# Kernel optimization log

Hardware: AMD Instinct MI355X
Metric: run time of the kernel (lower is better)

## Reference

```python
import jax, jax.numpy as jnp
import numpy as np

B, T, F, H = 256, 32, 128, 128
NUM_FILTERS, KH, KW, NUM_CLASSES = 64, 2, 2, 2
FLAT = NUM_FILTERS * (T - KH + 1) * (2 * F - KW + 1)  # 64*31*255 = 505920


def setup_inputs() -> dict:
    key = jax.random.key(0)
    ks = jax.random.split(key, 12)
    inp = {
        "X_nume": jax.random.normal(ks[0], (B, T, F), jnp.float32),
        "att_W": jax.random.uniform(ks[1], (F, H), jnp.float32),
        "att_U": jax.random.uniform(ks[2], (F, H), jnp.float32),
        "att_V": jax.random.uniform(ks[3], (H, 1), jnp.float32),
        "conv_w": jax.random.normal(ks[4], (NUM_FILTERS, 1, KH, KW), jnp.float32) * 0.5,
        "conv_b": jax.random.normal(ks[5], (NUM_FILTERS,), jnp.float32) * 0.1,
        "w1": jax.random.normal(ks[6], (FLAT, 256), jnp.float32) * (1.0 / np.sqrt(FLAT)),
        "b1": jnp.zeros((256,), jnp.float32),
        "w2": jax.random.normal(ks[7], (256, 32), jnp.float32) * (1.0 / np.sqrt(256)),
        "b2": jnp.zeros((32,), jnp.float32),
        "w3": jax.random.normal(ks[8], (32, NUM_CLASSES), jnp.float32) * (1.0 / np.sqrt(32)),
        "b3": jnp.zeros((NUM_CLASSES,), jnp.float32),
    }
    return inp


def reference(X_nume, att_W, att_U, att_V, conv_w, conv_b, w1, b1, w2, b2, w3, b3):
    X = X_nume  # [B, T, F]
    # --- additive attention, fully batched (replaces O(T^2) python loops) ---
    xw = jnp.einsum("btf,fh->bth", X, att_W)  # query proj [B,T,H]
    xu = jnp.einsum("btf,fh->bth", X, att_U)  # key proj   [B,T,H]
    # e[b,i,j] = V^T tanh(x_i W + x_j U)
    scores = jnp.squeeze(jnp.tanh(xw[:, :, None, :] + xu[:, None, :, :]) @ att_V, -1)  # [B,T,T]
    alpha = jax.nn.softmax(scores, axis=-1)  # softmax over j (includes diagonal)
    # context excludes j == i (original skips j == index AFTER softmax)
    mask = 1.0 - jnp.eye(T, dtype=X.dtype)
    c = jnp.einsum("bij,bjf->bif", alpha * mask, X)  # [B,T,F]
    feat = jnp.concatenate([X, c], axis=-1)  # [B,T,2F]
    # --- conv ---
    conv_in = feat[:, None, :, :]  # [B,1,T,2F]
    conv = jax.lax.conv_general_dilated(
        conv_in, conv_w, window_strides=(1, 1), padding="VALID",
        dimension_numbers=("NCHW", "OIHW", "NCHW"))
    conv = jax.nn.relu(conv + conv_b[None, :, None, None])  # [B,64,T-1,2F-1]
    # --- MLP head ---
    flat = conv.reshape(conv.shape[0], -1)
    h = jax.nn.relu(flat @ w1 + b1)
    h = jax.nn.relu(h @ w2 + b2)
    return h @ w3 + b3
```

## Files before the change

### kernel.cpp

```cpp
#include <hip/hip_runtime.h>
#include <hip/hip_bf16.h>

#define B_ 256
#define T_ 32
#define F_ 128
#define H_ 128
#define NF 64
#define OH 31
#define OW 255
#define POS_TOTAL (OH*OW)
#define N1 256
#define KT 248

typedef __attribute__((ext_vector_type(8))) short bf16x8;
typedef __attribute__((ext_vector_type(4))) float f32x4;

__device__ __forceinline__ unsigned int cvtpk(float lo, float hi) {
    unsigned int r;
    asm("v_cvt_pk_bf16_f32 %0, %1, %2" : "=v"(r) : "v"(lo), "v"(hi));
    return r;
}

__global__ __launch_bounds__(256) void k_attn(
    const float* __restrict__ X, const float* __restrict__ W,
    const float* __restrict__ U, const float* __restrict__ V,
    float* __restrict__ featL)
{
    __shared__ float Xs[T_][F_];
    __shared__ float xw[T_][H_];
    __shared__ float xu[T_][H_];
    __shared__ float sc[T_][T_];
    __shared__ float Vs[H_];

    const int b = blockIdx.x;
    const int t = threadIdx.x;
    const float* Xb = X + (size_t)b * T_ * F_;

    for (int idx = t; idx < T_*F_; idx += 256) ((float*)Xs)[idx] = Xb[idx];
    if (t < H_) Vs[t] = V[t];
    __syncthreads();

    {
        const int h = t & 127, half = t >> 7;
        float aw[16], au[16];
        #pragma unroll
        for (int r = 0; r < 16; r++) { aw[r] = 0.f; au[r] = 0.f; }
        for (int f = 0; f < F_; f++) {
            const float wv = W[f*H_ + h];
            const float uv = U[f*H_ + h];
            #pragma unroll
            for (int r = 0; r < 16; r++) {
                const float xv = Xs[half*16 + r][f];
                aw[r] += xv * wv;
                au[r] += xv * uv;
            }
        }
        #pragma unroll
        for (int r = 0; r < 16; r++) {
            xw[half*16 + r][h] = aw[r];
            xu[half*16 + r][h] = au[r];
        }
    }
    __syncthreads();

    {
        const int i = t >> 3;
        const int j0 = (t & 7) * 4;
        float s0 = 0.f, s1 = 0.f, s2 = 0.f, s3 = 0.f;
        for (int h = 0; h < H_; h++) {
            const float xwv = xw[i][h];
            const float vv  = Vs[h];
            s0 += tanhf(xwv + xu[j0+0][h]) * vv;
            s1 += tanhf(xwv + xu[j0+1][h]) * vv;
            s2 += tanhf(xwv + xu[j0+2][h]) * vv;
            s3 += tanhf(xwv + xu[j0+3][h]) * vv;
        }
        sc[i][j0+0] = s0; sc[i][j0+1] = s1; sc[i][j0+2] = s2; sc[i][j0+3] = s3;
    }
    __syncthreads();

    if (t < T_) {
        float m = -1e30f;
        #pragma unroll
        for (int j = 0; j < T_; j++) m = fmaxf(m, sc[t][j]);
        float sum = 0.f;
        #pragma unroll
        for (int j = 0; j < T_; j++) sum += expf(sc[t][j] - m);
        const float inv = 1.f / sum;
        #pragma unroll
        for (int j = 0; j < T_; j++) {
            const float a = expf(sc[t][j] - m) * inv;
            sc[t][j] = (j == t) ? 0.f : a;
        }
    }
    __syncthreads();

    for (int idx = t; idx < T_*F_; idx += 256) {
        const int row = idx >> 7, f = idx & 127;
        float acc = 0.f;
        #pragma unroll
        for (int j = 0; j < T_; j++) acc += sc[row][j] * Xs[j][f];
        float* fr = featL + (size_t)b*8192 + row*256;
        fr[f]       = Xs[row][f];
        fr[128 + f] = acc;
    }
}

__global__ __launch_bounds__(256) void k_tr(
    const float* __restrict__ src, float* __restrict__ dst)
{
    __shared__ float tile[32][33];
    const int rc0 = blockIdx.x * 32;
    const int b0  = blockIdx.y * 32;
    const int tx = threadIdx.x & 31;
    const int ty = threadIdx.x >> 5;
    #pragma unroll
    for (int r = 0; r < 32; r += 8)
        tile[ty + r][tx] = src[(size_t)(b0 + ty + r)*8192 + rc0 + tx];
    __syncthreads();
    #pragma unroll
    for (int r = 0; r < 32; r += 8)
        dst[(size_t)(rc0 + ty + r)*256 + b0 + tx] = tile[tx][ty + r];
}

__global__ __launch_bounds__(512, 2) void k_gemm1(
    const float* __restrict__ featT, const float* __restrict__ cw,
    const float* __restrict__ cb, const float* __restrict__ w1,
    float* __restrict__ partial)
{
    __shared__ unsigned short As[2][256*64];
    __shared__ unsigned short Ws[2][256*64];
    __shared__ float cwL[256];
    __shared__ float cbL[64];

    const int t  = threadIdx.x;
    const int kt = blockIdx.x;
    const int y  = kt >> 3;
    const int x0 = (kt & 7) * 32;

    if (t < 256) cwL[t] = cw[t];
    if (t < 64)  cbL[t] = cb[t];

    const int rm = t & 255;
    const int ph = t >> 8;
    const int r0 = (t & 15) * 4;
    const int c0 = (t >> 4) * 8;
    const int lane = t & 63, wid = t >> 6;
    const int wm = (wid >> 2) * 128;
    const int wn = (wid & 3) * 64;
    const int fr = lane & 15, fq = lane >> 4;

    f32x4 acc[8][4];
    #pragma unroll
    for (int i = 0; i < 8; i++)
        #pragma unroll
        for (int j = 0; j < 4; j++)
            acc[i][j] = (f32x4){0.f, 0.f, 0.f, 0.f};

    float topv[17], botv[17];
    #pragma unroll
    for (int i = 0; i < 17; i++) {
        int xc = x0 + ph*16 + i; if (xc > 255) xc = 255;
        topv[i] = featT[((size_t)(y*256 + xc))*256 + rm];
        botv[i] = featT[((size_t)((y+1)*256 + xc))*256 + rm];
    }

    float wvf[4][8];

#define W_LOADS(S)                                                             \
    {                                                                          \
        const int fl_ = r0 >> 5;                                               \
        const int f_  = 2*(S) + fl_;                                           \
        _Pragma("unroll")                                                      \
        for (int jj = 0; jj < 4; jj++) {                                       \
            int xc_ = x0 + (r0 & 31) + jj; if (xc_ > 254) xc_ = 254;           \
            const float* wp_ = w1 + ((size_t)(f_*POS_TOTAL + y*255 + xc_))*N1  \
                                  + c0;                                        \
            *(float4*)&wvf[jj][0] = *(const float4*)&wp_[0];                   \
            *(float4*)&wvf[jj][4] = *(const float4*)&wp_[4];                   \
        }                                                                      \
    }

#define STAGE(BUF, S)                                                          \
    {                                                                          \
        _Pragma("unroll")                                                      \
        for (int i = 0; i < 8; i++) {                                          \
            const int n_ = c0 + i;                                             \
            uint2 v_;                                                          \
            v_.x = cvtpk(wvf[0][i], wvf[1][i]);                                \
            v_.y = cvtpk(wvf[2][i], wvf[3][i]);                                \
            const int blk_ = (r0 >> 3) ^ (n_ & 7);                             \
            *(uint2*)&Ws[BUF][n_*64 + blk_*8 + (r0 & 7)] = v_;                 \
        }                                                                      \
        _Pragma("unroll")                                                      \
        for (int fl = 0; fl < 2; fl++) {                                       \
            const int f_ = 2*(S) + fl;                                         \
            const float4 cc_ = *(const float4*)&cwL[f_*4];                     \
            const float cbv_ = cbL[f_];                                        \
            unsigned int pk_[4];                                               \
            _Pragma("unroll")                                                  \
            for (int i2 = 0; i2 < 8; i2++) {                                   \
                const int i0 = 2*i2, i1 = 2*i2 + 1;                            \
                float v0_ = topv[i0]*cc_.x + topv[i0+1]*cc_.y                  \
                          + botv[i0]*cc_.z + botv[i0+1]*cc_.w + cbv_;          \
                float v1_ = topv[i1]*cc_.x + topv[i1+1]*cc_.y                  \
                          + botv[i1]*cc_.z + botv[i1+1]*cc_.w + cbv_;          \
                v0_ = (x0 + ph*16 + i0 < 255) ? fmaxf(v0_, 0.f) : 0.f;         \
                v1_ = (x0 + ph*16 + i1 < 255) ? fmaxf(v1_, 0.f) : 0.f;         \
                pk_[i2 & 3] = cvtpk(v0_, v1_);                                 \
                if ((i2 & 3) == 3) {                                           \
                    const int kb_ = fl*4 + ph*2 + (i2 >> 2);                   \
                    *(uint4*)&As[BUF][rm*64 + ((kb_ ^ (rm & 7))*8)]            \
                        = *(uint4*)&pk_[0];                                    \
                }                                                              \
            }                                                                  \
        }                                                                      \
    }

    W_LOADS(0);
    __syncthreads();
    STAGE(0, 0);
    asm volatile("s_waitcnt lgkmcnt(0)" ::: "memory");
    __builtin_amdgcn_s_barrier();

    #pragma unroll 1
    for (int s = 0; s < 32; s++) {
        const int cur = s & 1;
        if (s < 31) W_LOADS(s + 1);

        __builtin_amdgcn_s_setprio(1);
        #pragma unroll
        for (int kc = 0; kc < 2; kc++) {
            const int sw = ((kc*4 + fq) ^ (fr & 7)) * 8;
            bf16x8 bf_[4];
            #pragma unroll
            for (int ng = 0; ng < 4; ng++)
                bf_[ng] = *(const bf16x8*)&Ws[cur][(wn + ng*16 + fr)*64 + sw];
            #pragma unroll
            for (int mg = 0; mg < 8; mg++) {
                const bf16x8 af_ =
                    *(const bf16x8*)&As[cur][(wm + mg*16 + fr)*64 + sw];
                #pragma unroll
                for (int ng = 0; ng < 4; ng++)
                    acc[mg][ng] = __builtin_amdgcn_mfma_f32_16x16x32_bf16(
                        af_, bf_[ng], acc[mg][ng], 0, 0, 0);
            }
        }
        __builtin_amdgcn_s_setprio(0);

        if (s < 31) STAGE(cur ^ 1, s + 1);
        asm volatile("s_waitcnt lgkmcnt(0)" ::: "memory");
        __builtin_amdgcn_s_barrier();
    }

    float* pp = partial + (size_t)kt * (256*N1);
    #pragma unroll
    for (int mg = 0; mg < 8; mg++)
        #pragma unroll
        for (int ng = 0; ng < 4; ng++) {
            const int col = wn + ng*16 + fr;
            #pragma unroll
            for (int j = 0; j < 4; j++) {
                const int row = wm + mg*16 + fq*4 + j;
                pp[(size_t)row*N1 + col] = acc[mg][ng][j];
            }
        }
#undef W_LOADS
#undef STAGE
}

__global__ __launch_bounds__(256) void k_head(
    const float* __restrict__ partial,
    const float* __restrict__ b1, const float* __restrict__ w2,
    const float* __restrict__ b2, const float* __restrict__ w3,
    const float* __restrict__ b3, float* __restrict__ out)
{
    __shared__ float h1s[256];
    __shared__ float h2s[32];
    const int b = blockIdx.x, t = threadIdx.x;

    const float* pb = partial + (size_t)b*N1 + t;
    float s0 = 0.f, s1 = 0.f, s2 = 0.f, s3 = 0.f;
    #pragma unroll 2
    for (int kt = 0; kt < KT; kt += 4) {
        s0 += pb[(size_t)(kt+0)*65536];
        s1 += pb[(size_t)(kt+1)*65536];
        s2 += pb[(size_t)(kt+2)*65536];
        s3 += pb[(size_t)(kt+3)*65536];
    }
    h1s[t] = fmaxf(b1[t] + ((s0+s1)+(s2+s3)), 0.f);
    __syncthreads();

    if (t < 32) {
        float s2v = b2[t];
        for (int i = 0; i < 256; i++) s2v += h1s[i] * w2[i*32 + t];
        h2s[t] = fmaxf(s2v, 0.f);
    }
    __syncthreads();

    if (t < 2) {
        float s3v = b3[t];
        #pragma unroll
        for (int i = 0; i < 32; i++) s3v += h2s[i] * w3[i*2 + t];
        out[b*2 + t] = s3v;
    }
}

extern "C" void kernel_launch(void* const* d_in, const int* in_sizes, int n_in,
                              void* d_out, int out_size, void* d_ws, size_t ws_size,
                              hipStream_t stream) {
    const float* X    = (const float*)d_in[0];
    const float* attW = (const float*)d_in[1];
    const float* attU = (const float*)d_in[2];
    const float* attV = (const float*)d_in[3];
    const float* cw   = (const float*)d_in[4];
    const float* cb   = (const float*)d_in[5];
    const float* w1   = (const float*)d_in[6];
    const float* b1   = (const float*)d_in[7];
    const float* w2   = (const float*)d_in[8];
    const float* b2   = (const float*)d_in[9];
    const float* w3   = (const float*)d_in[10];
    const float* b3   = (const float*)d_in[11];
    float* out = (float*)d_out;

    float* featL   = (float*)d_ws;
    float* featT   = (float*)((char*)d_ws + (8u<<20));
    float* partial = (float*)((char*)d_ws + (16u<<20));

    k_attn <<<dim3(B_),       dim3(256), 0, stream>>>(X, attW, attU, attV, featL);
    k_tr   <<<dim3(256, 8),   dim3(256), 0, stream>>>(featL, featT);
    k_gemm1<<<dim3(KT),       dim3(512), 0, stream>>>(featT, cw, cb, w1, partial);
    k_head <<<dim3(B_),       dim3(256), 0, stream>>>(partial, b1, w2, b2, w3, b3, out);
}
```

Baseline: 269.5 us.

## Load w1 fragments straight into registers and drop the LDS weight buffer

```diff
diff --git a/kernel.cpp b/kernel.cpp
--- a/kernel.cpp
+++ b/kernel.cpp
@@ -129,7 +129,6 @@
     float* __restrict__ partial)
 {
     __shared__ unsigned short As[2][256*64];
-    __shared__ unsigned short Ws[2][256*64];
     __shared__ float cwL[256];
     __shared__ float cbL[64];
 
@@ -143,19 +142,16 @@
 
     const int rm = t & 255;
     const int ph = t >> 8;
-    const int r0 = (t & 15) * 4;
-    const int c0 = (t >> 4) * 8;
     const int lane = t & 63, wid = t >> 6;
-    const int wm = (wid >> 2) * 128;
-    const int wn = (wid & 3) * 64;
+    const int wn = wid * 32;
     const int fr = lane & 15, fq = lane >> 4;
 
-    f32x4 acc[8][4];
-    #pragma unroll
-    for (int i = 0; i < 8; i++)
-        #pragma unroll
-        for (int j = 0; j < 4; j++)
-            acc[i][j] = (f32x4){0.f, 0.f, 0.f, 0.f};
+    f32x4 acc[16][2];
+    #pragma unroll
+    for (int i = 0; i < 16; i++) {
+        acc[i][0] = (f32x4){0.f, 0.f, 0.f, 0.f};
+        acc[i][1] = (f32x4){0.f, 0.f, 0.f, 0.f};
+    }
 
     float topv[17], botv[17];
     #pragma unroll
@@ -165,33 +161,30 @@
         botv[i] = featT[((size_t)((y+1)*256 + xc))*256 + rm];
     }
 
-    float wvf[4][8];
-
-#define W_LOADS(S)                                                             \
+    int poff[8];
+    #pragma unroll
+    for (int j = 0; j < 8; j++) {
+        int xc = x0 + fq*8 + j; if (xc > 254) xc = 254;
+        poff[j] = (y*255 + xc)*N1 + wn + fr;
+    }
+
+    float wv[2][2][8];
+
+#define WLOAD(S)                                                               \
     {                                                                          \
-        const int fl_ = r0 >> 5;                                               \
-        const int f_  = 2*(S) + fl_;                                           \
         _Pragma("unroll")                                                      \
-        for (int jj = 0; jj < 4; jj++) {                                       \
-            int xc_ = x0 + (r0 & 31) + jj; if (xc_ > 254) xc_ = 254;           \
-            const float* wp_ = w1 + ((size_t)(f_*POS_TOTAL + y*255 + xc_))*N1  \
-                                  + c0;                                        \
-            *(float4*)&wvf[jj][0] = *(const float4*)&wp_[0];                   \
-            *(float4*)&wvf[jj][4] = *(const float4*)&wp_[4];                   \
+        for (int kc = 0; kc < 2; kc++) {                                       \
+            const float* wf_ = w1 + (size_t)(2*(S) + kc) * (POS_TOTAL*N1);     \
+            _Pragma("unroll")                                                  \
+            for (int ng = 0; ng < 2; ng++)                                     \
+                _Pragma("unroll")                                              \
+                for (int j = 0; j < 8; j++)                                    \
+                    wv[kc][ng][j] = wf_[poff[j] + ng*16];                      \
         }                                                                      \
     }
 
 #define STAGE(BUF, S)                                                          \
     {                                                                          \
-        _Pragma("unroll")                                                      \
-        for (int i = 0; i < 8; i++) {                                          \
-            const int n_ = c0 + i;                                             \
-            uint2 v_;                                                          \
-            v_.x = cvtpk(wvf[0][i], wvf[1][i]);                                \
-            v_.y = cvtpk(wvf[2][i], wvf[3][i]);                                \
-            const int blk_ = (r0 >> 3) ^ (n_ & 7);                             \
-            *(uint2*)&Ws[BUF][n_*64 + blk_*8 + (r0 & 7)] = v_;                 \
-        }                                                                      \
         _Pragma("unroll")                                                      \
         for (int fl = 0; fl < 2; fl++) {                                       \
             const int f_ = 2*(S) + fl;                                         \
@@ -217,7 +210,7 @@
         }                                                                      \
     }
 
-    W_LOADS(0);
+    WLOAD(0);
     __syncthreads();
     STAGE(0, 0);
     asm volatile("s_waitcnt lgkmcnt(0)" ::: "memory");
@@ -226,24 +219,32 @@
     #pragma unroll 1
     for (int s = 0; s < 32; s++) {
         const int cur = s & 1;
-        if (s < 31) W_LOADS(s + 1);
+
+        bf16x8 bf[2][2];
+        #pragma unroll
+        for (int kc = 0; kc < 2; kc++)
+            #pragma unroll
+            for (int ng = 0; ng < 2; ng++) {
+                unsigned int* bu = (unsigned int*)&bf[kc][ng];
+                #pragma unroll
+                for (int q = 0; q < 4; q++)
+                    bu[q] = cvtpk(wv[kc][ng][2*q], wv[kc][ng][2*q+1]);
+            }
+
+        if (s < 31) WLOAD(s + 1);
 
         __builtin_amdgcn_s_setprio(1);
         #pragma unroll
         for (int kc = 0; kc < 2; kc++) {
             const int sw = ((kc*4 + fq) ^ (fr & 7)) * 8;
-            bf16x8 bf_[4];
             #pragma unroll
-            for (int ng = 0; ng < 4; ng++)
-                bf_[ng] = *(const bf16x8*)&Ws[cur][(wn + ng*16 + fr)*64 + sw];
-            #pragma unroll
-            for (int mg = 0; mg < 8; mg++) {
-                const bf16x8 af_ =
-                    *(const bf16x8*)&As[cur][(wm + mg*16 + fr)*64 + sw];
-                #pragma unroll
-                for (int ng = 0; ng < 4; ng++)
-                    acc[mg][ng] = __builtin_amdgcn_mfma_f32_16x16x32_bf16(
-                        af_, bf_[ng], acc[mg][ng], 0, 0, 0);
+            for (int mg = 0; mg < 16; mg++) {
+                const bf16x8 af =
+                    *(const bf16x8*)&As[cur][(mg*16 + fr)*64 + sw];
+                acc[mg][0] = __builtin_amdgcn_mfma_f32_16x16x32_bf16(
+                    af, bf[kc][0], acc[mg][0], 0, 0, 0);
+                acc[mg][1] = __builtin_amdgcn_mfma_f32_16x16x32_bf16(
+                    af, bf[kc][1], acc[mg][1], 0, 0, 0);
             }
         }
         __builtin_amdgcn_s_setprio(0);
@@ -255,17 +256,17 @@
 
     float* pp = partial + (size_t)kt * (256*N1);
     #pragma unroll
-    for (int mg = 0; mg < 8; mg++)
-        #pragma unroll
-        for (int ng = 0; ng < 4; ng++) {
+    for (int mg = 0; mg < 16; mg++)
+        #pragma unroll
+        for (int ng = 0; ng < 2; ng++) {
             const int col = wn + ng*16 + fr;
             #pragma unroll
             for (int j = 0; j < 4; j++) {
-                const int row = wm + mg*16 + fq*4 + j;
+                const int row = mg*16 + fq*4 + j;
                 pp[(size_t)row*N1 + col] = acc[mg][ng][j];
             }
         }
-#undef W_LOADS
+#undef WLOAD
 #undef STAGE
 }
 
```

Result: faster. 260.7 us, median of 2 (-3.3%).

## Prefetch w1 two stages ahead with double register buffers; pack conv inputs as bf16

Applied to the files above, without the earlier changes.

```diff
diff --git a/kernel.cpp b/kernel.cpp
--- a/kernel.cpp
+++ b/kernel.cpp
@@ -20,6 +20,9 @@
     asm("v_cvt_pk_bf16_f32 %0, %1, %2" : "=v"(r) : "v"(lo), "v"(hi));
     return r;
 }
+#define PLO(u) __uint_as_float((u) << 16)
+#define PHI(u) __uint_as_float((u) & 0xffff0000u)
+#define PAT(arr, i) (((i) & 1) ? PHI(arr[(i) >> 1]) : PLO(arr[(i) >> 1]))
 
 __global__ __launch_bounds__(256) void k_attn(
     const float* __restrict__ X, const float* __restrict__ W,
@@ -157,17 +160,20 @@
         for (int j = 0; j < 4; j++)
             acc[i][j] = (f32x4){0.f, 0.f, 0.f, 0.f};
 
-    float topv[17], botv[17];
-    #pragma unroll
-    for (int i = 0; i < 17; i++) {
-        int xc = x0 + ph*16 + i; if (xc > 255) xc = 255;
-        topv[i] = featT[((size_t)(y*256 + xc))*256 + rm];
-        botv[i] = featT[((size_t)((y+1)*256 + xc))*256 + rm];
-    }
-
-    float wvf[4][8];
-
-#define W_LOADS(S)                                                             \
+    unsigned int tp[9], bp[9];
+    #pragma unroll
+    for (int q = 0; q < 9; q++) {
+        int xa = x0 + ph*16 + 2*q;     if (xa > 255) xa = 255;
+        int xb = x0 + ph*16 + 2*q + 1; if (xb > 255) xb = 255;
+        tp[q] = cvtpk(featT[((size_t)(y*256 + xa))*256 + rm],
+                      featT[((size_t)(y*256 + xb))*256 + rm]);
+        bp[q] = cvtpk(featT[((size_t)((y+1)*256 + xa))*256 + rm],
+                      featT[((size_t)((y+1)*256 + xb))*256 + rm]);
+    }
+
+    float wvA[4][8], wvB[4][8];
+
+#define W_LOADS(DST, S)                                                        \
     {                                                                          \
         const int fl_ = r0 >> 5;                                               \
         const int f_  = 2*(S) + fl_;                                           \
@@ -176,19 +182,19 @@
             int xc_ = x0 + (r0 & 31) + jj; if (xc_ > 254) xc_ = 254;           \
             const float* wp_ = w1 + ((size_t)(f_*POS_TOTAL + y*255 + xc_))*N1  \
                                   + c0;                                        \
-            *(float4*)&wvf[jj][0] = *(const float4*)&wp_[0];                   \
-            *(float4*)&wvf[jj][4] = *(const float4*)&wp_[4];                   \
+            *(float4*)&DST[jj][0] = *(const float4*)&wp_[0];                   \
+            *(float4*)&DST[jj][4] = *(const float4*)&wp_[4];                   \
         }                                                                      \
     }
 
-#define STAGE(BUF, S)                                                          \
+#define STAGE(BUF, S, WSRC)                                                    \
     {                                                                          \
         _Pragma("unroll")                                                      \
         for (int i = 0; i < 8; i++) {                                          \
             const int n_ = c0 + i;                                             \
             uint2 v_;                                                          \
-            v_.x = cvtpk(wvf[0][i], wvf[1][i]);                                \
-            v_.y = cvtpk(wvf[2][i], wvf[3][i]);                                \
+            v_.x = cvtpk(WSRC[0][i], WSRC[1][i]);                              \
+            v_.y = cvtpk(WSRC[2][i], WSRC[3][i]);                              \
             const int blk_ = (r0 >> 3) ^ (n_ & 7);                             \
             *(uint2*)&Ws[BUF][n_*64 + blk_*8 + (r0 & 7)] = v_;                 \
         }                                                                      \
@@ -201,10 +207,10 @@
             _Pragma("unroll")                                                  \
             for (int i2 = 0; i2 < 8; i2++) {                                   \
                 const int i0 = 2*i2, i1 = 2*i2 + 1;                            \
-                float v0_ = topv[i0]*cc_.x + topv[i0+1]*cc_.y                  \
-                          + botv[i0]*cc_.z + botv[i0+1]*cc_.w + cbv_;          \
-                float v1_ = topv[i1]*cc_.x + topv[i1+1]*cc_.y                  \
-                          + botv[i1]*cc_.z + botv[i1+1]*cc_.w + cbv_;          \
+                float v0_ = PAT(tp,i0)*cc_.x + PAT(tp,i0+1)*cc_.y              \
+                          + PAT(bp,i0)*cc_.z + PAT(bp,i0+1)*cc_.w + cbv_;      \
+                float v1_ = PAT(tp,i1)*cc_.x + PAT(tp,i1+1)*cc_.y              \
+                          + PAT(bp,i1)*cc_.z + PAT(bp,i1+1)*cc_.w + cbv_;      \
                 v0_ = (x0 + ph*16 + i0 < 255) ? fmaxf(v0_, 0.f) : 0.f;         \
                 v1_ = (x0 + ph*16 + i1 < 255) ? fmaxf(v1_, 0.f) : 0.f;         \
                 pk_[i2 & 3] = cvtpk(v0_, v1_);                                 \
@@ -217,38 +223,48 @@
         }                                                                      \
     }
 
-    W_LOADS(0);
-    __syncthreads();
-    STAGE(0, 0);
+#define DO_MFMA(BUF)                                                           \
+    {                                                                          \
+        __builtin_amdgcn_s_setprio(1);                                         \
+        _Pragma("unroll")                                                      \
+        for (int kc = 0; kc < 2; kc++) {                                       \
+            const int sw = ((kc*4 + fq) ^ (fr & 7)) * 8;                       \
+            bf16x8 bf_[4];                                                     \
+            _Pragma("unroll")                                                  \
+            for (int ng = 0; ng < 4; ng++)                                     \
+                bf_[ng] = *(const bf16x8*)&Ws[BUF][(wn + ng*16 + fr)*64 + sw]; \
+            _Pragma("unroll")                                                  \
+            for (int mg = 0; mg < 8; mg++) {                                   \
+                const bf16x8 af_ =                                             \
+                    *(const bf16x8*)&As[BUF][(wm + mg*16 + fr)*64 + sw];       \
+                _Pragma("unroll")                                              \
+                for (int ng = 0; ng < 4; ng++)                                 \
+                    acc[mg][ng] = __builtin_amdgcn_mfma_f32_16x16x32_bf16(     \
+                        af_, bf_[ng], acc[mg][ng], 0, 0, 0);                   \
+            }                                                                  \
+        }                                                                      \
+        __builtin_amdgcn_s_setprio(0);                                         \
+    }
+
+    W_LOADS(wvA, 0);
+    W_LOADS(wvB, 1);
+    __syncthreads();
+    STAGE(0, 0, wvA);
     asm volatile("s_waitcnt lgkmcnt(0)" ::: "memory");
     __builtin_amdgcn_s_barrier();
 
     #pragma unroll 1
     for (int s = 0; s < 32; s++) {
         const int cur = s & 1;
-        if (s < 31) W_LOADS(s + 1);
-
-        __builtin_amdgcn_s_setprio(1);
-        #pragma unroll
-        for (int kc = 0; kc < 2; kc++) {
-            const int sw = ((kc*4 + fq) ^ (fr & 7)) * 8;
-            bf16x8 bf_[4];
-            #pragma unroll
-            for (int ng = 0; ng < 4; ng++)
-                bf_[ng] = *(const bf16x8*)&Ws[cur][(wn + ng*16 + fr)*64 + sw];
-            #pragma unroll
-            for (int mg = 0; mg < 8; mg++) {
-                const bf16x8 af_ =
-                    *(const bf16x8*)&As[cur][(wm + mg*16 + fr)*64 + sw];
-                #pragma unroll
-                for (int ng = 0; ng < 4; ng++)
-                    acc[mg][ng] = __builtin_amdgcn_mfma_f32_16x16x32_bf16(
-                        af_, bf_[ng], acc[mg][ng], 0, 0, 0);
-            }
-        }
-        __builtin_amdgcn_s_setprio(0);
-
-        if (s < 31) STAGE(cur ^ 1, s + 1);
+        if (s + 2 < 32) {
+            if (cur == 0) W_LOADS(wvA, s + 2)
+            else          W_LOADS(wvB, s + 2)
+        }
+        DO_MFMA(cur);
+        if (s + 1 < 32) {
+            if (cur == 0) STAGE(cur ^ 1, s + 1, wvB)
+            else          STAGE(cur ^ 1, s + 1, wvA)
+        }
         asm volatile("s_waitcnt lgkmcnt(0)" ::: "memory");
         __builtin_amdgcn_s_barrier();
     }
@@ -267,6 +283,7 @@
         }
 #undef W_LOADS
 #undef STAGE
+#undef DO_MFMA
 }
 
 __global__ __launch_bounds__(256) void k_head(
```

Result: slower. 372.7 us (+38.3%).
